# Kernel optimization log

Measured on AMD Instinct MI355X. Metric: run time of the kernel, lower is better.

Reference implementation:

```python
import jax, jax.numpy as jnp
import numpy as np

B, NN, HL = 64, 64, 50
IN_DIM, POS_DIM, ATT_DIM = 384, 64, 256
NEWS_DIM = IN_DIM + POS_DIM  # 448


def setup_inputs() -> dict:
    key = jax.random.key(0)
    ks = jax.random.split(key, 8)
    pos_emb = jax.random.uniform(ks[3], (100, POS_DIM), jnp.float32, -0.1, 0.1)
    pos_emb = pos_emb.at[0].set(0.0)  # initialize() zeros row 0
    return {
        "log_vec": jax.random.normal(ks[0], (B, HL, IN_DIM), jnp.float32),
        "log_mask": jax.random.randint(ks[1], (B, HL), 0, 2, jnp.int32),
        "news_vec": jax.random.normal(ks[2], (B, NN, IN_DIM), jnp.float32),
        "pos_emb": pos_emb,
        "W1": jax.random.normal(ks[4], (ATT_DIM, 2 * NEWS_DIM), jnp.float32) * 0.02,
        "b1": jnp.zeros((ATT_DIM,), jnp.float32),
        "W2": jax.random.normal(ks[5], (1, ATT_DIM), jnp.float32) * 0.02,
        "b2": jnp.zeros((1,), jnp.float32),
    }


def reference(log_vec, log_mask, news_vec, pos_emb, W1, b1, W2, b2):
    b, nn_ = news_vec.shape[:2]
    hl = log_mask.shape[1]
    # append position embeddings (row 0 for candidates, rows 1..hl for history)
    nf = jnp.concatenate(
        [news_vec, jnp.broadcast_to(pos_emb[0], (b, nn_, POS_DIM))], axis=-1)   # (B,NN,ND)
    lf = jnp.concatenate(
        [log_vec, jnp.broadcast_to(pos_emb[1:hl + 1], (b, hl, POS_DIM))], axis=-1)  # (B,HL,ND)
    # affine1(cat[news, log]) == news @ Wn^T + log @ Wl^T + b1 (avoids concat)
    Wn, Wl = W1[:, :NEWS_DIM], W1[:, NEWS_DIM:]
    pn = jnp.einsum('bnd,ad->bna', nf, Wn)   # (B,NN,A)
    pl = jnp.einsum('bhd,ad->bha', lf, Wl)   # (B,HL,A)
    h = jnp.tanh(pn[:, :, None, :] + pl[:, None, :, :] + b1)  # (B,NN,HL,A)
    logits = jnp.einsum('bnha,a->bnh', h, W2[0]) + b2[0]      # (B,NN,HL)
    logits = jnp.where(log_mask[:, None, :] == 0, jnp.float32(-1e9), logits)
    attn = jax.nn.softmax(logits, axis=2)
    user_log_vecs = jnp.einsum('bnh,bhd->bnd', attn, lf)      # (B,NN,ND)
    return user_log_vecs, nf
```

## Files before the change

kernel.cpp:

```cpp
#include <hip/hip_runtime.h>
#include <math.h>

typedef unsigned short u16;
typedef unsigned int   u32;

#define B_       64
#define NN_      64
#define HL_      50
#define IN_DIM   384
#define POS_DIM  64
#define ATT_DIM  256
#define NEWS_DIM 448

typedef __attribute__((ext_vector_type(8))) short short8;
typedef __attribute__((ext_vector_type(4))) float f32x4;

#if __has_builtin(__builtin_amdgcn_exp2f)
#define EXP2F(x) __builtin_amdgcn_exp2f(x)
#else
#define EXP2F(x) exp2f(x)
#endif
#if __has_builtin(__builtin_amdgcn_rcpf)
#define RCPF(x) __builtin_amdgcn_rcpf(x)
#else
#define RCPF(x) (1.0f/(x))
#endif

__device__ __forceinline__ u16 f2bf(float f) {
    union { float f; u32 i; } v; v.f = f;
    u32 r = v.i + 0x7fffu + ((v.i >> 16) & 1u);
    return (u16)(r >> 16);
}
__device__ __forceinline__ float bf2f(u16 u) {
    union { u32 i; float f; } v; v.i = ((u32)u) << 16; return v.f;
}
__device__ __forceinline__ uint2 pack4(float4 v) {
    return make_uint2((u32)f2bf(v.x) | ((u32)f2bf(v.y) << 16),
                      (u32)f2bf(v.z) | ((u32)f2bf(v.w) << 16));
}
__device__ __forceinline__ float fast_tanh(float x) {
    float e = EXP2F(x * 2.88539008f);
    return 1.0f - 2.0f * RCPF(1.0f + e);
}

__global__ __launch_bounds__(256) void prep_k(
    const float* __restrict__ W1, const float* __restrict__ newsv,
    const float* __restrict__ logv, const float* __restrict__ pos,
    u16* __restrict__ Wbf, u16* __restrict__ nv_bf, u16* __restrict__ lf_bf,
    float* __restrict__ nf)
{
    u32 bid = blockIdx.x, tid = threadIdx.x;
    if (bid < 2936u) {
        u32 x = bid & 7u, j = bid >> 3;
        if (j < 192u) {
            u32 idx = j * 256u + tid;
            u32 r = 512u * x + idx / 96u, d4 = idx % 96u;
            float4 v = *(const float4*)(newsv + (size_t)r * IN_DIM + d4 * 4u);
            *(uint2*)(nv_bf + (size_t)r * IN_DIM + d4 * 4u) = pack4(v);
            *(float4*)(nf + (size_t)r * NEWS_DIM + d4 * 4u) = v;
        } else if (j < 342u) {
            u32 idx = (j - 192u) * 256u + tid;
            u32 r = 400u * x + idx / 96u, d4 = idx % 96u;
            float4 v = *(const float4*)(logv + (size_t)r * IN_DIM + d4 * 4u);
            *(uint2*)(lf_bf + (size_t)r * NEWS_DIM + d4 * 4u) = pack4(v);
        } else {
            u32 idx = (j - 342u) * 256u + tid;
            u32 r = 400u * x + idx / 16u, d4 = idx % 16u;
            u32 h = r % HL_;
            float4 v = *(const float4*)(pos + (size_t)(1u + h) * POS_DIM + d4 * 4u);
            *(uint2*)(lf_bf + (size_t)r * NEWS_DIM + IN_DIM + d4 * 4u) = pack4(v);
        }
        return;
    }
    bid -= 2936u;
    if (bid < 224u) {
        u32 i = bid * 256u + tid;
        float4 v = *(const float4*)(W1 + (size_t)i * 4u);
        *(uint2*)(Wbf + (size_t)i * 4u) = pack4(v);
        return;
    }
    bid -= 224u;
    {
        u32 i = bid * 256u + tid;
        u32 r = i / 16u, d4 = i % 16u;
        *(float4*)(nf + (size_t)r * NEWS_DIM + IN_DIM + d4 * 4u) =
            make_float4(0.f, 0.f, 0.f, 0.f);
    }
}

__global__ __launch_bounds__(64) void gemm_k(
    const u16* __restrict__ nv_bf, const u16* __restrict__ lf_bf,
    const u16* __restrict__ Wbf, const float* __restrict__ b1,
    float* __restrict__ pn, float* __restrict__ plT)
{
    int bid = blockIdx.x;
    int lane = threadIdx.x;
    int m = lane & 15, q = lane >> 4;
    int x = bid & 7, j = bid >> 3;
    bool is_pn = j < 128;
    int r0, c0, lda, koff, klen;
    const u16* A;
    if (is_pn) {
        int b = x * 8 + (j >> 4);
        r0 = b * 64 + ((j >> 2) & 3) * 16;
        c0 = (j & 3) * 64;
        A = nv_bf; lda = IN_DIM;   koff = 0;        klen = IN_DIM;
    } else {
        int j2 = j - 128;
        r0 = 400 * x + (j2 >> 2) * 16;
        c0 = (j2 & 3) * 64;
        A = lf_bf; lda = NEWS_DIM; koff = NEWS_DIM; klen = NEWS_DIM;
    }

    f32x4 acc[4];
#pragma unroll
    for (int b = 0; b < 4; b++) acc[b] = (f32x4){0.f, 0.f, 0.f, 0.f};

    const u16* Ap = A + (size_t)(r0 + m) * lda + q * 8;
    const u16* Wp = Wbf + (size_t)(c0 + m) * (2 * NEWS_DIM) + koff + q * 8;

    for (int k = 0; k < klen; k += 32) {
        short8 af, wf[4];
        af = *(const short8*)(Ap + k);
#pragma unroll
        for (int ct = 0; ct < 4; ct++) wf[ct] = *(const short8*)(Wp + ct * 16 * (2 * NEWS_DIM) + k);
#pragma unroll
        for (int ct = 0; ct < 4; ct++)
            acc[ct] = __builtin_amdgcn_mfma_f32_16x16x32_bf16(af, wf[ct], acc[ct], 0, 0, 0);
    }
#pragma unroll
    for (int ct = 0; ct < 4; ct++)
#pragma unroll
        for (int i = 0; i < 4; i++) {
            int gr = r0 + q * 4 + i;
            int gc = c0 + ct * 16 + m;
            float v = acc[ct][i];
            if (is_pn) {
                pn[(size_t)gr * ATT_DIM + gc] = v + b1[gc];
            } else {
                int bb = gr / HL_, hh = gr - bb * HL_;
                plT[(size_t)(bb * ATT_DIM + gc) * HL_ + hh] = v;
            }
        }
}

__global__ __launch_bounds__(256) void attn_out_k(
    const float* __restrict__ pn, const float* __restrict__ plT,
    const float* __restrict__ w2, const int* __restrict__ lmask,
    const u16* __restrict__ lf_bf, float* __restrict__ out)
{
    __shared__ float pl_s[4][800];
    __shared__ float part[4][4][64];
    __shared__ float at4[64][4];
    int lane = threadIdx.x & 63;
    int wid = __builtin_amdgcn_readfirstlane((int)(threadIdx.x >> 6));
    int x     = blockIdx.x & 7;
    int local = blockIdx.x >> 3;
    int b     = x * 8 + (local >> 4);
    int n0    = (local & 15) * 4;
    int g0    = b * 64 + n0;
    int n_hl  = (lane < HL_) ? lane : (HL_ - 1);

    int a0 = wid * 64;
    const float* pr0 = pn + (size_t)(g0 + 0) * ATT_DIM + a0;
    const float* pr1 = pn + (size_t)(g0 + 1) * ATT_DIM + a0;
    const float* pr2 = pn + (size_t)(g0 + 2) * ATT_DIM + a0;
    const float* pr3 = pn + (size_t)(g0 + 3) * ATT_DIM + a0;
    const float* w2o = w2 + a0;
    const float4* src4 = (const float4*)(plT + ((size_t)b * ATT_DIM + a0) * HL_);
    float* pls = pl_s[wid];

    float c0 = 0.f, c1 = 0.f, c2 = 0.f, c3 = 0.f;
    float d0 = 0.f, d1 = 0.f, d2 = 0.f, d3 = 0.f;

    float4 s0 = src4[lane];
    float4 s1 = src4[lane + 64];
    float4 s2 = src4[lane + 128];
    float4 s3 = (lane < 8) ? src4[lane + 192] : make_float4(0.f, 0.f, 0.f, 0.f);

    for (int c = 0; c < 4; c++) {
        *(float4*)&pls[4 * lane]         = s0;
        *(float4*)&pls[4 * (lane + 64)]  = s1;
        *(float4*)&pls[4 * (lane + 128)] = s2;
        if (lane < 8) *(float4*)&pls[4 * (lane + 192)] = s3;
        if (c < 3) {
            const float4* nx = src4 + (c + 1) * 200;
            s0 = nx[lane];
            s1 = nx[lane + 64];
            s2 = nx[lane + 128];
            if (lane < 8) s3 = nx[lane + 192];
        }
        int ab = c * 16;
#pragma unroll 4
        for (int i = 0; i < 16; i += 4) {
            int a = ab + i;
            float4 w4 = *(const float4*)(w2o + a);
            float4 pA = *(const float4*)(pr0 + a);
            float4 pB = *(const float4*)(pr1 + a);
            float4 pC = *(const float4*)(pr2 + a);
            float4 pD = *(const float4*)(pr3 + a);
            float l0 = pls[(i + 0) * HL_ + n_hl];
            float l1 = pls[(i + 1) * HL_ + n_hl];
            float l2 = pls[(i + 2) * HL_ + n_hl];
            float l3 = pls[(i + 3) * HL_ + n_hl];
            c0 = __builtin_fmaf(fast_tanh(pA.x + l0), w4.x, c0);
            d0 = __builtin_fmaf(fast_tanh(pA.y + l1), w4.y, d0);
            c0 = __builtin_fmaf(fast_tanh(pA.z + l2), w4.z, c0);
            d0 = __builtin_fmaf(fast_tanh(pA.w + l3), w4.w, d0);
            c1 = __builtin_fmaf(fast_tanh(pB.x + l0), w4.x, c1);
            d1 = __builtin_fmaf(fast_tanh(pB.y + l1), w4.y, d1);
            c1 = __builtin_fmaf(fast_tanh(pB.z + l2), w4.z, c1);
            d1 = __builtin_fmaf(fast_tanh(pB.w + l3), w4.w, d1);
            c2 = __builtin_fmaf(fast_tanh(pC.x + l0), w4.x, c2);
            d2 = __builtin_fmaf(fast_tanh(pC.y + l1), w4.y, d2);
            c2 = __builtin_fmaf(fast_tanh(pC.z + l2), w4.z, c2);
            d2 = __builtin_fmaf(fast_tanh(pC.w + l3), w4.w, d2);
            c3 = __builtin_fmaf(fast_tanh(pD.x + l0), w4.x, c3);
            d3 = __builtin_fmaf(fast_tanh(pD.y + l1), w4.y, d3);
            c3 = __builtin_fmaf(fast_tanh(pD.z + l2), w4.z, c3);
            d3 = __builtin_fmaf(fast_tanh(pD.w + l3), w4.w, d3);
        }
    }
    part[wid][0][lane] = c0 + d0;
    part[wid][1][lane] = c1 + d1;
    part[wid][2][lane] = c2 + d2;
    part[wid][3][lane] = c3 + d3;
    __syncthreads();

    float acc = (part[0][wid][lane] + part[1][wid][lane])
              + (part[2][wid][lane] + part[3][wid][lane]);
    int mv = (lane < HL_) ? lmask[b * HL_ + lane] : 0;
    float logit = mv ? acc : -1e9f;
    float mx = logit;
#pragma unroll
    for (int o = 32; o > 0; o >>= 1) mx = fmaxf(mx, __shfl_xor(mx, o));
    float e = EXP2F((logit - mx) * 1.44269504f);
    float s = e;
#pragma unroll
    for (int o = 32; o > 0; o >>= 1) s += __shfl_xor(s, o);
    at4[lane][wid] = e * RCPF(s);
    __syncthreads();

    int l56 = (lane < 56) ? lane : 55;
    int k   = wid * 56 + l56;
    const u32* lfb32 = (const u32*)(lf_bf + (size_t)b * HL_ * NEWS_DIM);
    float q00 = 0.f, q01 = 0.f, q10 = 0.f, q11 = 0.f;
    float q20 = 0.f, q21 = 0.f, q30 = 0.f, q31 = 0.f;
    for (int h = 0; h < HL_; h++) {
        float4 av = *(const float4*)at4[h];
        u32 v = lfb32[h * (NEWS_DIM / 2) + k];
        float f0 = bf2f((u16)v), f1 = bf2f((u16)(v >> 16));
        q00 = fmaf(av.x, f0, q00);  q01 = fmaf(av.x, f1, q01);
        q10 = fmaf(av.y, f0, q10);  q11 = fmaf(av.y, f1, q11);
        q20 = fmaf(av.z, f0, q20);  q21 = fmaf(av.z, f1, q21);
        q30 = fmaf(av.w, f0, q30);  q31 = fmaf(av.w, f1, q31);
    }
    if (lane < 56) {
        float* o0 = out + (size_t)g0 * NEWS_DIM + 2 * k;
        *(float2*)(o0)                = make_float2(q00, q01);
        *(float2*)(o0 + NEWS_DIM)     = make_float2(q10, q11);
        *(float2*)(o0 + 2 * NEWS_DIM) = make_float2(q20, q21);
        *(float2*)(o0 + 3 * NEWS_DIM) = make_float2(q30, q31);
    }
}

extern "C" void kernel_launch(void* const* d_in, const int* in_sizes, int n_in,
                              void* d_out, int out_size, void* d_ws, size_t ws_size,
                              hipStream_t stream) {
    const float* logv  = (const float*)d_in[0];
    const int*   lmask = (const int*)d_in[1];
    const float* newsv = (const float*)d_in[2];
    const float* pos   = (const float*)d_in[3];
    const float* W1    = (const float*)d_in[4];
    const float* b1    = (const float*)d_in[5];
    const float* w2    = (const float*)d_in[6];

    float* out = (float*)d_out;
    float* nf  = out + (size_t)B_ * NN_ * NEWS_DIM;

    char* ws = (char*)d_ws;
    u16*   lf_bf = (u16*)(ws + 0);
    u16*   Wbf   = (u16*)(ws + 2867200);
    u16*   nv_bf = (u16*)(ws + 3325952);
    float* pn    = (float*)(ws + 6471680);
    float* plT   = (float*)(ws + 10665984);

    prep_k    <<<3416, 256, 0, stream>>>(W1, newsv, logv, pos,
                                         Wbf, nv_bf, lf_bf, nf);
    gemm_k    <<<1824, 64, 0, stream>>>(nv_bf, lf_bf, Wbf, b1, pn, plT);
    attn_out_k<<<1024, 256, 0, stream>>>(pn, plT, w2, lmask, lf_bf, out);
}
```

Measured before the change: 122.9 us.

## Fuse bf16 conversion prep kernel into GEMM and read fp32 inputs directly

Removes the separate prep kernel that converted inputs and W1 to bf16 in workspace. The GEMM now loads fp32 inputs and weights and converts them in registers with v_cvt_pk_bf16_f32, and extra blocks of the GEMM launch write the nf output. The attention-output stage reads fp32 log vectors and position embeddings directly instead of the bf16 copy. This saves one launch and a workspace round trip, but every GEMM tile now reloads twice the bytes and redoes the conversion, with W1 converted repeatedly across blocks.

```diff
diff --git a/kernel.cpp b/kernel.cpp
--- a/kernel.cpp
+++ b/kernel.cpp
@@ -26,104 +26,87 @@
 #define RCPF(x) (1.0f/(x))
 #endif
 
-__device__ __forceinline__ u16 f2bf(float f) {
-    union { float f; u32 i; } v; v.f = f;
-    u32 r = v.i + 0x7fffu + ((v.i >> 16) & 1u);
-    return (u16)(r >> 16);
-}
 __device__ __forceinline__ float bf2f(u16 u) {
     union { u32 i; float f; } v; v.i = ((u32)u) << 16; return v.f;
 }
-__device__ __forceinline__ uint2 pack4(float4 v) {
-    return make_uint2((u32)f2bf(v.x) | ((u32)f2bf(v.y) << 16),
-                      (u32)f2bf(v.z) | ((u32)f2bf(v.w) << 16));
+__device__ __forceinline__ short8 cvt8(float4 a, float4 b) {
+    union { short8 s; u32 u[4]; } r;
+    asm("v_cvt_pk_bf16_f32 %0, %1, %2" : "=v"(r.u[0]) : "v"(a.x), "v"(a.y));
+    asm("v_cvt_pk_bf16_f32 %0, %1, %2" : "=v"(r.u[1]) : "v"(a.z), "v"(a.w));
+    asm("v_cvt_pk_bf16_f32 %0, %1, %2" : "=v"(r.u[2]) : "v"(b.x), "v"(b.y));
+    asm("v_cvt_pk_bf16_f32 %0, %1, %2" : "=v"(r.u[3]) : "v"(b.z), "v"(b.w));
+    return r.s;
 }
 __device__ __forceinline__ float fast_tanh(float x) {
     float e = EXP2F(x * 2.88539008f);
     return 1.0f - 2.0f * RCPF(1.0f + e);
 }
 
-__global__ __launch_bounds__(256) void prep_k(
-    const float* __restrict__ W1, const float* __restrict__ newsv,
-    const float* __restrict__ logv, const float* __restrict__ pos,
-    u16* __restrict__ Wbf, u16* __restrict__ nv_bf, u16* __restrict__ lf_bf,
-    float* __restrict__ nf)
-{
-    u32 bid = blockIdx.x, tid = threadIdx.x;
-    if (bid < 2936u) {
-        u32 x = bid & 7u, j = bid >> 3;
-        if (j < 192u) {
-            u32 idx = j * 256u + tid;
-            u32 r = 512u * x + idx / 96u, d4 = idx % 96u;
-            float4 v = *(const float4*)(newsv + (size_t)r * IN_DIM + d4 * 4u);
-            *(uint2*)(nv_bf + (size_t)r * IN_DIM + d4 * 4u) = pack4(v);
-            *(float4*)(nf + (size_t)r * NEWS_DIM + d4 * 4u) = v;
-        } else if (j < 342u) {
-            u32 idx = (j - 192u) * 256u + tid;
-            u32 r = 400u * x + idx / 96u, d4 = idx % 96u;
-            float4 v = *(const float4*)(logv + (size_t)r * IN_DIM + d4 * 4u);
-            *(uint2*)(lf_bf + (size_t)r * NEWS_DIM + d4 * 4u) = pack4(v);
-        } else {
-            u32 idx = (j - 342u) * 256u + tid;
-            u32 r = 400u * x + idx / 16u, d4 = idx % 16u;
-            u32 h = r % HL_;
-            float4 v = *(const float4*)(pos + (size_t)(1u + h) * POS_DIM + d4 * 4u);
-            *(uint2*)(lf_bf + (size_t)r * NEWS_DIM + IN_DIM + d4 * 4u) = pack4(v);
-        }
-        return;
-    }
-    bid -= 2936u;
-    if (bid < 224u) {
-        u32 i = bid * 256u + tid;
-        float4 v = *(const float4*)(W1 + (size_t)i * 4u);
-        *(uint2*)(Wbf + (size_t)i * 4u) = pack4(v);
-        return;
-    }
-    bid -= 224u;
-    {
-        u32 i = bid * 256u + tid;
-        u32 r = i / 16u, d4 = i % 16u;
-        *(float4*)(nf + (size_t)r * NEWS_DIM + IN_DIM + d4 * 4u) =
-            make_float4(0.f, 0.f, 0.f, 0.f);
-    }
-}
-
 __global__ __launch_bounds__(64) void gemm_k(
-    const u16* __restrict__ nv_bf, const u16* __restrict__ lf_bf,
-    const u16* __restrict__ Wbf, const float* __restrict__ b1,
-    float* __restrict__ pn, float* __restrict__ plT)
+    const float* __restrict__ newsv, const float* __restrict__ logv,
+    const float* __restrict__ pos, const float* __restrict__ W1,
+    const float* __restrict__ b1,
+    float* __restrict__ pn, float* __restrict__ plT, float* __restrict__ nf)
 {
     int bid = blockIdx.x;
     int lane = threadIdx.x;
+    if (bid >= 1824) {
+        int j = bid - 1824;
+#pragma unroll
+        for (int t = 0; t < 7; t++) {
+            int idx  = t * 64 + lane;
+            int row4 = idx / 112, col4 = idx - row4 * 112;
+            int r    = j * 4 + row4;
+            float4 v = (col4 < 96)
+                ? *(const float4*)(newsv + (size_t)r * IN_DIM + col4 * 4)
+                : make_float4(0.f, 0.f, 0.f, 0.f);
+            *(float4*)(nf + (size_t)r * NEWS_DIM + col4 * 4) = v;
+        }
+        return;
+    }
+
     int m = lane & 15, q = lane >> 4;
     int x = bid & 7, j = bid >> 3;
     bool is_pn = j < 128;
-    int r0, c0, lda, koff, klen;
-    const u16* A;
+    int r0, c0, koff, klen;
     if (is_pn) {
         int b = x * 8 + (j >> 4);
         r0 = b * 64 + ((j >> 2) & 3) * 16;
         c0 = (j & 3) * 64;
-        A = nv_bf; lda = IN_DIM;   koff = 0;        klen = IN_DIM;
+        koff = 0;        klen = IN_DIM;
     } else {
         int j2 = j - 128;
         r0 = 400 * x + (j2 >> 2) * 16;
         c0 = (j2 & 3) * 64;
-        A = lf_bf; lda = NEWS_DIM; koff = NEWS_DIM; klen = NEWS_DIM;
-    }
+        koff = NEWS_DIM; klen = NEWS_DIM;
+    }
+
+    int row = r0 + m;
+    const float* Af;
+    const float* Ap2 = nullptr;
+    if (is_pn) {
+        Af = newsv + (size_t)row * IN_DIM + q * 8;
+    } else {
+        int hh = row % 50;
+        Af  = logv + (size_t)row * IN_DIM + q * 8;
+        Ap2 = pos + (size_t)(1 + hh) * POS_DIM - IN_DIM + q * 8;
+    }
+    const float* Wp = W1 + (size_t)(c0 + m) * (2 * NEWS_DIM) + koff + q * 8;
 
     f32x4 acc[4];
 #pragma unroll
     for (int b = 0; b < 4; b++) acc[b] = (f32x4){0.f, 0.f, 0.f, 0.f};
 
-    const u16* Ap = A + (size_t)(r0 + m) * lda + q * 8;
-    const u16* Wp = Wbf + (size_t)(c0 + m) * (2 * NEWS_DIM) + koff + q * 8;
-
     for (int k = 0; k < klen; k += 32) {
-        short8 af, wf[4];
-        af = *(const short8*)(Ap + k);
-#pragma unroll
-        for (int ct = 0; ct < 4; ct++) wf[ct] = *(const short8*)(Wp + ct * 16 * (2 * NEWS_DIM) + k);
+        int e0 = q * 8 + k;
+        const float* as = (!is_pn && e0 >= IN_DIM) ? Ap2 : Af;
+        short8 af = cvt8(*(const float4*)(as + k), *(const float4*)(as + k + 4));
+        short8 wf[4];
+#pragma unroll
+        for (int ct = 0; ct < 4; ct++) {
+            const float* ws_ = Wp + (size_t)ct * 16 * (2 * NEWS_DIM);
+            wf[ct] = cvt8(*(const float4*)(ws_ + k), *(const float4*)(ws_ + k + 4));
+        }
 #pragma unroll
         for (int ct = 0; ct < 4; ct++)
             acc[ct] = __builtin_amdgcn_mfma_f32_16x16x32_bf16(af, wf[ct], acc[ct], 0, 0, 0);
@@ -147,7 +130,8 @@
 __global__ __launch_bounds__(256) void attn_out_k(
     const float* __restrict__ pn, const float* __restrict__ plT,
     const float* __restrict__ w2, const int* __restrict__ lmask,
-    const u16* __restrict__ lf_bf, float* __restrict__ out)
+    const float* __restrict__ logv, const float* __restrict__ pos,
+    float* __restrict__ out)
 {
     __shared__ float pl_s[4][800];
     __shared__ float part[4][4][64];
@@ -243,17 +227,19 @@
 
     int l56 = (lane < 56) ? lane : 55;
     int k   = wid * 56 + l56;
-    const u32* lfb32 = (const u32*)(lf_bf + (size_t)b * HL_ * NEWS_DIM);
+    const float* lrow = logv + (size_t)b * (HL_ * IN_DIM) + 2 * k;
+    const float* prow = pos + POS_DIM + 2 * k - IN_DIM;
+    bool usep = (k >= 192);
     float q00 = 0.f, q01 = 0.f, q10 = 0.f, q11 = 0.f;
     float q20 = 0.f, q21 = 0.f, q30 = 0.f, q31 = 0.f;
     for (int h = 0; h < HL_; h++) {
         float4 av = *(const float4*)at4[h];
-        u32 v = lfb32[h * (NEWS_DIM / 2) + k];
-        float f0 = bf2f((u16)v), f1 = bf2f((u16)(v >> 16));
-        q00 = fmaf(av.x, f0, q00);  q01 = fmaf(av.x, f1, q01);
-        q10 = fmaf(av.y, f0, q10);  q11 = fmaf(av.y, f1, q11);
-        q20 = fmaf(av.z, f0, q20);  q21 = fmaf(av.z, f1, q21);
-        q30 = fmaf(av.w, f0, q30);  q31 = fmaf(av.w, f1, q31);
+        float2 v = usep ? *(const float2*)(prow + h * POS_DIM)
+                        : *(const float2*)(lrow + (size_t)h * IN_DIM);
+        q00 = fmaf(av.x, v.x, q00);  q01 = fmaf(av.x, v.y, q01);
+        q10 = fmaf(av.y, v.x, q10);  q11 = fmaf(av.y, v.y, q11);
+        q20 = fmaf(av.z, v.x, q20);  q21 = fmaf(av.z, v.y, q21);
+        q30 = fmaf(av.w, v.x, q30);  q31 = fmaf(av.w, v.y, q31);
     }
     if (lane < 56) {
         float* o0 = out + (size_t)g0 * NEWS_DIM + 2 * k;
@@ -279,14 +265,9 @@
     float* nf  = out + (size_t)B_ * NN_ * NEWS_DIM;
 
     char* ws = (char*)d_ws;
-    u16*   lf_bf = (u16*)(ws + 0);
-    u16*   Wbf   = (u16*)(ws + 2867200);
-    u16*   nv_bf = (u16*)(ws + 3325952);
-    float* pn    = (float*)(ws + 6471680);
-    float* plT   = (float*)(ws + 10665984);
-
-    prep_k    <<<3416, 256, 0, stream>>>(W1, newsv, logv, pos,
-                                         Wbf, nv_bf, lf_bf, nf);
-    gemm_k    <<<1824, 64, 0, stream>>>(nv_bf, lf_bf, Wbf, b1, pn, plT);
-    attn_out_k<<<1024, 256, 0, stream>>>(pn, plT, w2, lmask, lf_bf, out);
-}
+    float* pn  = (float*)(ws + 0);
+    float* plT = (float*)(ws + 4194304);
+
+    gemm_k    <<<2848, 64, 0, stream>>>(newsv, logv, pos, W1, b1, pn, plT, nf);
+    attn_out_k<<<1024, 256, 0, stream>>>(pn, plT, w2, lmask, logv, pos, out);
+}
```

Result: slower. 134.1 us (+9.1%).
